# Kernel optimization log

Hardware: AMD Instinct MI355X
Metric: run time of the kernel (lower is better)

The kernel has to match this reference:

```python
import jax, jax.numpy as jnp
import numpy as np

B, L, D, H = 2, 2048, 2048, 16
DH = D // H  # 128 per-head dim
EPS = 1e-5


def setup_inputs() -> dict:
    key = jax.random.key(0)
    ks = jax.random.split(key, 6)
    s = 0.02  # xavier-ish init scale with gain 2**-2.5
    return {
        "hidden_states": jax.random.normal(ks[0], (B, L, D), jnp.float32),
        "Wq": jax.random.normal(ks[1], (D, D), jnp.float32) * s,
        "Wk": jax.random.normal(ks[2], (D, D), jnp.float32) * s,
        "Wv": jax.random.normal(ks[3], (D, D), jnp.float32) * s,
        "Wb": jax.random.normal(ks[4], (D, H), jnp.float32) * s,
        "o_norm_weight": jnp.ones((DH,), jnp.float32),
        "Wo": jax.random.normal(ks[5], (D, D), jnp.float32) * s,
    }


def _delta_rule(q, k, v, beta):
    """Recurrent delta-rule linear attention.
    q,k,v: [B,H,L,Dh]; beta: [B,H,L]. Math identical to fused_chunk_delta_rule.
    S_t = S_{t-1} + k_t (beta_t * (v_t - S_{t-1}^T k_t))^T ;  o_t = S_t^T q_t
    """
    def step(S, inp):
        qt, kt, vt, bt = inp  # [B,H,Dh],[B,H,Dh],[B,H,Dh],[B,H]
        v_pred = jnp.einsum('bhk,bhkv->bhv', kt, S)
        delta = (vt - v_pred) * bt[..., None]
        S = S + kt[..., None] * delta[:, :, None, :]
        ot = jnp.einsum('bhk,bhkv->bhv', qt, S)
        return S, ot

    xs = (q.transpose(2, 0, 1, 3), k.transpose(2, 0, 1, 3),
          v.transpose(2, 0, 1, 3), beta.transpose(2, 0, 1))
    S0 = jnp.zeros(q.shape[:2] + (q.shape[-1], v.shape[-1]), q.dtype)
    _, o = jax.lax.scan(step, S0, xs)  # o: [L,B,H,Dh]
    return o.transpose(1, 2, 0, 3)  # [B,H,L,Dh]


def reference(hidden_states, Wq, Wk, Wv, Wb, o_norm_weight, Wo):
    b, l, d = hidden_states.shape
    h = Wb.shape[1]
    dh = d // h

    q = hidden_states @ Wq
    k = hidden_states @ Wk
    v = jax.nn.silu(hidden_states @ Wv)

    def heads(x):
        return x.reshape(b, l, h, dh).transpose(0, 2, 1, 3)  # b h l d

    q, k, v = heads(q), heads(k), heads(v)

    # qk_norm = 'l2' (torch F.normalize with eps clamp)
    def l2n(x):
        n = jnp.sqrt(jnp.sum(x * x, axis=-1, keepdims=True))
        return x / jnp.maximum(n, 1e-12)

    q, k = l2n(q), l2n(k)
    q = q * (dh ** -0.5)  # fla delta-rule default scale

    beta = jax.nn.sigmoid(hidden_states @ Wb).transpose(0, 2, 1)  # b h l

    o = _delta_rule(q, k, v, beta)  # b h l dh
    o = o.transpose(0, 2, 1, 3)  # b l h dh

    # RMSNorm over head_v_dim
    o = o * jax.lax.rsqrt(jnp.mean(o * o, axis=-1, keepdims=True) + EPS)
    o = o * o_norm_weight

    return o.reshape(b, l, d) @ Wo
```

## Files before the change

### kernel.cpp

```cpp
#include <hip/hip_runtime.h>
#include <hip/hip_bf16.h>
#include <cstdint>

#define DEV static __device__ __forceinline__

typedef unsigned short u16;
typedef unsigned int u32;
typedef __attribute__((ext_vector_type(8))) short short8;
typedef __attribute__((ext_vector_type(4))) float f32x4;

constexpr int Bn = 2, Ln = 2048, Dn = 2048, Hn = 16;
constexpr int Mrows = Bn * Ln;
constexpr int CHK = 64, NCK = Ln / CHK;
constexpr int NCHUNKS = Bn * Hn * NCK;

DEV float b2f(u16 s) { union { float f; u32 u; } x; x.u = ((u32)s) << 16; return x.f; }
DEV u16 f2b(float f) {
  union { float f; u32 u; } x; x.f = f; u32 u = x.u;
  return (u16)((u + 0x7fffu + ((u >> 16) & 1u)) >> 16);
}

DEV void cp16(const void* g, void* l) {
  __builtin_amdgcn_global_load_lds(
      (const __attribute__((address_space(1))) u32*)(unsigned long long)(g),
      (__attribute__((address_space(3))) u32*)(unsigned long long)(l), 16, 0, 0);
}

DEV f32x4 mfma16(short8 a, short8 b, f32x4 c) {
  return __builtin_amdgcn_mfma_f32_16x16x32_bf16(a, b, c, 0, 0, 0);
}

__global__ void k_cvt(const float* __restrict__ src, u16* __restrict__ dst, int n8) {
  int i = blockIdx.x * blockDim.x + threadIdx.x;
  if (i >= n8) return;
  const float4* s4 = (const float4*)(src + (size_t)i * 8);
  float4 a = s4[0], b = s4[1];
  u16 o[8] = {f2b(a.x), f2b(a.y), f2b(a.z), f2b(a.w), f2b(b.x), f2b(b.y), f2b(b.z), f2b(b.w)};
  *(short8*)(dst + (size_t)i * 8) = *(short8*)o;
}

struct TransArgs {
  const float* src[5]; u16* dst[5]; int rows[5]; int cols[5];
};
__global__ void k_trans(TransArgs t) {
  __shared__ u16 tile[32][33];
  int z = blockIdx.z;
  const float* src = t.src[z]; u16* dst = t.dst[z];
  int rows = t.rows[z], cols = t.cols[z];
  int r0 = blockIdx.y * 32, c0 = blockIdx.x * 32;
  if (r0 >= rows || c0 >= cols) return;
  int tx = threadIdx.x, ty = threadIdx.y;
  for (int i = ty; i < 32; i += 8) {
    int r = r0 + i, c = c0 + tx;
    if (r < rows && c < cols) tile[i][tx] = f2b(src[(size_t)r * cols + c]);
  }
  __syncthreads();
  for (int i = ty; i < 32; i += 8) {
    int r = c0 + i, c = r0 + tx;
    if (r < cols && c < rows) dst[(size_t)r * rows + c] = tile[tx][i];
  }
}

__global__ __launch_bounds__(256) void k_beta(const u16* __restrict__ hs,
                                              const u16* __restrict__ WbT,
                                              float* __restrict__ beta_g) {
  int tid = threadIdx.x, wave = tid >> 6, lane = tid & 63, quad = lane >> 4, l15 = lane & 15;
  int tok0 = blockIdx.x * 64 + wave * 16;
  const u16* arow = hs + (size_t)(tok0 + l15) * Dn;
  const u16* brow = WbT + (size_t)l15 * Dn;
  f32x4 acc = {0.f, 0.f, 0.f, 0.f};
  for (int k = 0; k < Dn; k += 32) {
    short8 af = *(const short8*)&arow[k + quad * 8];
    short8 bf = *(const short8*)&brow[k + quad * 8];
    acc = mfma16(af, bf, acc);
  }
  int b = (blockIdx.x * 64) >> 11;
  int l = (blockIdx.x * 64 + wave * 16) & 2047;
#pragma unroll
  for (int r = 0; r < 4; r++) {
    beta_g[(size_t)(b * Hn + l15) * Ln + l + quad * 4 + r] = 1.f / (1.f + __expf(-acc[r]));
  }
}

struct GemmArgs {
  const u16* A; const u16* Bt; void* C; int epi;
  int f32out;
  int M, N, K;
};
__global__ __launch_bounds__(256) void k_gemm(GemmArgs g) {
  __shared__ u16 As[128 * 64];
  __shared__ u16 Bs[128 * 64];
  const u16* A = g.A; const u16* Bt = g.Bt;
  int epi = g.epi;
  int K = g.K, N = g.N;
  int tid = threadIdx.x, wave = tid >> 6, lane = tid & 63;
  int quad = lane >> 4, l15 = lane & 15;
  int m0 = blockIdx.y * 128, n0 = blockIdx.x * 128;
  int wm = (wave >> 1) * 64, wn = (wave & 1) * 64;
  f32x4 acc[4][4];
#pragma unroll
  for (int i = 0; i < 4; i++)
#pragma unroll
    for (int j = 0; j < 4; j++) acc[i][j] = (f32x4){0.f, 0.f, 0.f, 0.f};
  int scol = ((lane & 7) ^ (lane >> 3)) * 8;
  const u16* Ag = A + (size_t)(m0 + wave * 32 + (lane >> 3)) * K + scol;
  const u16* Bg = Bt + (size_t)(n0 + wave * 32 + (lane >> 3)) * K + scol;
  u16* Al = &As[wave * 32 * 64];
  u16* Bl = &Bs[wave * 32 * 64];
  int sw8 = l15 & 7;
  for (int k0 = 0; k0 < K; k0 += 64) {
#pragma unroll
    for (int t = 0; t < 4; t++) {
      cp16(Ag + k0 + t * 8 * K, Al + t * 8 * 64);
      cp16(Bg + k0 + t * 8 * K, Bl + t * 8 * 64);
    }
    __syncthreads();
#pragma unroll
    for (int kk = 0; kk < 64; kk += 32) {
      int sl = (((kk >> 3) + quad) ^ sw8) * 8;
      short8 af[4], bf[4];
#pragma unroll
      for (int i = 0; i < 4; i++) af[i] = *(const short8*)&As[(wm + i * 16 + l15) * 64 + sl];
#pragma unroll
      for (int i = 0; i < 4; i++) bf[i] = *(const short8*)&Bs[(wn + i * 16 + l15) * 64 + sl];
#pragma unroll
      for (int i = 0; i < 4; i++)
#pragma unroll
        for (int j = 0; j < 4; j++) acc[i][j] = mfma16(af[i], bf[j], acc[i][j]);
    }
    __syncthreads();
  }
#pragma unroll
  for (int i = 0; i < 4; i++)
#pragma unroll
    for (int j = 0; j < 4; j++) {
      int row = m0 + wm + i * 16 + quad * 4;
      int col = n0 + wn + j * 16 + l15;
#pragma unroll
      for (int r = 0; r < 4; r++) {
        float v = acc[i][j][r];
        if (epi == 1) v = v / (1.f + __expf(-v));
        if (g.f32out) ((float*)g.C)[(size_t)(row + r) * N + col] = v;
        else ((u16*)g.C)[(size_t)(row + r) * N + col] = f2b(v);
      }
    }
}

struct Gemm2Args { const u16* A; const u16* Bt; u16* C; int K; };

__global__ __launch_bounds__(512, 2) void k_gemm2(Gemm2Args g) {
  __shared__ u16 ldsbuf[61440];
  const char* LB = (const char*)ldsbuf;
  const int K = g.K, NT = K / 64;
  const size_t Kb = (size_t)K * 2;
  int tid = threadIdx.x, wave = tid >> 6, lane = tid & 63;
  int quad = lane >> 4, l15 = lane & 15;
  int wm = wave >> 2, wn = wave & 3;

  int bid = blockIdx.x;
  int wg = (bid & 7) * 32 + (bid >> 3);
  int by = wg >> 4, bx = wg & 15;
  int m0 = by * 256, n0f = bx * 384;

  int r0 = tid >> 2;
  int cby = (((tid & 3) ^ ((tid >> 3) & 3)) * 16);
  const char* gA = (const char*)g.A + (size_t)(m0 + r0) * Kb + cby;
  const char* gB = (const char*)g.Bt + (size_t)(n0f + r0) * Kb + cby;

  auto stageA = [&](int slot, int t, int kh) {
    const char* src = gA + (size_t)t * 128 + kh * 64;
    u16* dst = &ldsbuf[slot * 8192 + tid * 8];
    cp16(src, dst);
    cp16(src + (size_t)128 * Kb, dst + 4096);
  };
  auto stageB = [&](int slot, int t, int kh) {
    const char* src = gB + (size_t)t * 128 + kh * 64;
    u16* dst = &ldsbuf[24576 + slot * 12288 + tid * 8];
    cp16(src, dst);
    cp16(src + (size_t)128 * Kb, dst + 4096);
    cp16(src + (size_t)256 * Kb, dst + 8192);
  };

  f32x4 acc0[4][6], acc1[4][6];
#pragma unroll
  for (int i = 0; i < 4; i++)
#pragma unroll
    for (int j = 0; j < 6; j++) {
      acc0[i][j] = (f32x4){0.f, 0.f, 0.f, 0.f};
      acc1[i][j] = (f32x4){0.f, 0.f, 0.f, 0.f};
    }

  int rsw = (l15 >> 1) & 3;
  int rA = (wm * 128 + l15) * 64 + ((quad ^ rsw) * 16);
  int rB = (wn * 96 + l15) * 64 + ((quad ^ rsw) * 16);

  stageA(0, 0, 0);
  stageB(0, 0, 0);
  stageA(1, 0, 1);
  stageB(1, 0, 1);

  short8 bf[6];
  int u0 = 0;
  for (int t = 0; t < NT; ++t) {
    int u1 = u0 + 1; if (u1 == 3) u1 = 0;
    int u2 = u1 + 1; if (u2 == 3) u2 = 0;
    bool pf = (t + 1 < NT);
    const char* aK0 = LB + u0 * 16384;
    const char* aK1 = LB + u1 * 16384;
    const char* bK0 = LB + 49152 + u0 * 24576;
    const char* bK1 = LB + 49152 + u1 * 24576;

    asm volatile("s_waitcnt vmcnt(5)" ::: "memory");
    __builtin_amdgcn_s_barrier();
    __builtin_amdgcn_sched_barrier(0);
    if (pf) stageA(u2, t + 1, 0);
    {
      short8 av[4];
#pragma unroll
      for (int i = 0; i < 4; i++) av[i] = *(const short8*)(aK0 + rA + i * 1024);
#pragma unroll
      for (int j = 0; j < 6; j++) bf[j] = *(const short8*)(bK0 + rB + j * 1024);
      __builtin_amdgcn_s_setprio(1);
#pragma unroll
      for (int i = 0; i < 4; i++)
#pragma unroll
        for (int j = 0; j < 6; j++) acc0[i][j] = mfma16(av[i], bf[j], acc0[i][j]);
      __builtin_amdgcn_s_setprio(0);
    }

    asm volatile("s_waitcnt vmcnt(5)" ::: "memory");
    __builtin_amdgcn_s_barrier();
    __builtin_amdgcn_sched_barrier(0);
    if (pf) stageB(u2, t + 1, 0);
    {
      short8 av[4];
#pragma unroll
      for (int i = 0; i < 4; i++) av[i] = *(const short8*)(aK0 + rA + 4096 + i * 1024);
      __builtin_amdgcn_s_setprio(1);
#pragma unroll
      for (int i = 0; i < 4; i++)
#pragma unroll
        for (int j = 0; j < 6; j++) acc1[i][j] = mfma16(av[i], bf[j], acc1[i][j]);
      __builtin_amdgcn_s_setprio(0);
    }

    if (t == NT - 1) asm volatile("s_waitcnt vmcnt(0)" ::: "memory");
    else asm volatile("s_waitcnt vmcnt(5)" ::: "memory");
    __builtin_amdgcn_s_barrier();
    __builtin_amdgcn_sched_barrier(0);
    if (pf) stageA(u0, t + 1, 1);
    {
      short8 av[4];
#pragma unroll
      for (int i = 0; i < 4; i++) av[i] = *(const short8*)(aK1 + rA + i * 1024);
#pragma unroll
      for (int j = 0; j < 6; j++) bf[j] = *(const short8*)(bK1 + rB + j * 1024);
      __builtin_amdgcn_s_setprio(1);
#pragma unroll
      for (int i = 0; i < 4; i++)
#pragma unroll
        for (int j = 0; j < 6; j++) acc0[i][j] = mfma16(av[i], bf[j], acc0[i][j]);
      __builtin_amdgcn_s_setprio(0);
    }

    asm volatile("s_waitcnt vmcnt(5)" ::: "memory");
    __builtin_amdgcn_s_barrier();
    __builtin_amdgcn_sched_barrier(0);
    if (pf) stageB(u0, t + 1, 1);
    {
      short8 av[4];
#pragma unroll
      for (int i = 0; i < 4; i++) av[i] = *(const short8*)(aK1 + rA + 4096 + i * 1024);
      __builtin_amdgcn_s_setprio(1);
#pragma unroll
      for (int i = 0; i < 4; i++)
#pragma unroll
        for (int j = 0; j < 6; j++) acc1[i][j] = mfma16(av[i], bf[j], acc1[i][j]);
      __builtin_amdgcn_s_setprio(0);
    }

    u0 = u2;
  }

#pragma unroll
  for (int mq = 0; mq < 2; mq++) {
#pragma unroll
    for (int i = 0; i < 4; i++)
#pragma unroll
      for (int j = 0; j < 6; j++) {
        f32x4 a = mq ? acc1[i][j] : acc0[i][j];
        int row = m0 + wm * 128 + mq * 64 + i * 16 + quad * 4;
        int colg = n0f + wn * 96 + j * 16;
        int z = colg >> 11;
        u16* Cz = g.C + (size_t)z * ((size_t)Mrows * 2048);
        int col = (colg & 2047) + l15;
#pragma unroll
        for (int r = 0; r < 4; r++) {
          float v = a[r];
          if (z == 2) v = v / (1.f + __expf(-v));
          Cz[(size_t)(row + r) * 2048 + col] = f2b(v);
        }
      }
  }
}

__global__ void k_l2(u16* qn, u16* kn) {
  int tid = threadIdx.x, wave = tid >> 6, lane = tid & 63;
  size_t row = (size_t)blockIdx.x * 4 + wave;
  u16* p = (blockIdx.y ? kn : qn) + row * 128;
  u32 u = *(const u32*)&p[lane * 2];
  float x0 = b2f((u16)(u & 0xffff)), x1 = b2f((u16)(u >> 16));
  float ss = x0 * x0 + x1 * x1;
#pragma unroll
  for (int o = 32; o > 0; o >>= 1) ss += __shfl_xor(ss, o, 64);
  float sc = 1.f / fmaxf(sqrtf(ss), 1e-12f);
  if (blockIdx.y == 0) sc *= 0.08838834764831845f;
  u32 outv = (u32)f2b(x0 * sc) | ((u32)f2b(x1 * sc) << 16);
  *(u32*)&p[lane * 2] = outv;
}

constexpr int ST = 72;
__global__ __launch_bounds__(256, 4) void k_pre(
    const float* __restrict__ beta_g,
    const u16* __restrict__ qn, const u16* __restrict__ kn, const u16* __restrict__ vn,
    u16* __restrict__ W2g, u16* __restrict__ Ug, u16* __restrict__ Gg, u16* __restrict__ KTg) {
  __shared__ float beta_s[64];
  __shared__ u16 mats[4 * 64 * ST];
  int gid = blockIdx.x;
  int c = gid & 31, h = (gid >> 5) & 15, b = gid >> 9;
  int tid = threadIdx.x;
  int l0 = c * 64;

  if (tid < 64) beta_s[tid] = beta_g[(size_t)(b * Hn + h) * Ln + l0 + tid];
  __syncthreads();

  int wave = tid >> 6, lane = tid & 63, quad = lane >> 4, l15 = lane & 15;
  u16 *Br = mats, *Bc = mats + 64 * ST, *M0 = mats + 2 * 64 * ST, *M1 = mats + 3 * 64 * ST;

  {
    const u16* krowB = kn + (size_t)(b * Ln + l0 + wave * 16 + l15) * Dn + h * 128;
    short8 bfr[4];
#pragma unroll
    for (int s = 0; s < 4; s++) bfr[s] = *(const short8*)&krowB[quad * 8 + 32 * s];
#pragma unroll
    for (int mt = 0; mt < 4; ++mt) {
      const u16* arow_k = kn + (size_t)(b * Ln + l0 + mt * 16 + l15) * Dn + h * 128;
      const u16* arow_q = qn + (size_t)(b * Ln + l0 + mt * 16 + l15) * Dn + h * 128;
      f32x4 accA = {0.f, 0.f, 0.f, 0.f}, accG = {0.f, 0.f, 0.f, 0.f};
#pragma unroll
      for (int s = 0; s < 4; s++) {
        short8 ak = *(const short8*)&arow_k[quad * 8 + 32 * s];
        short8 aq = *(const short8*)&arow_q[quad * 8 + 32 * s];
        accA = mfma16(ak, bfr[s], accA);
        accG = mfma16(aq, bfr[s], accG);
      }
      int t = wave * 16 + l15;
#pragma unroll
      for (int r = 0; r < 4; r++) {
        int i = mt * 16 + quad * 4 + r;
        u16 nb = f2b((t < i) ? -beta_s[i] * accA[r] : 0.f);
        Br[i * ST + t] = nb;
        Bc[t * ST + i] = nb;
        M0[i * ST + t] = (t == i) ? f2b(1.f) : nb;
        Gg[(size_t)gid * 4096 + (size_t)i * 64 + t] = f2b((t <= i) ? accG[r] : 0.f);
      }
    }
  }
  __syncthreads();

  u16 *Mc = M0, *Mn = M1;
#pragma unroll
  for (int it = 0; it < 5; ++it) {
    const int tT = (it < 3) ? 0 : ((it == 3) ? 1 : 2);
    const int tI = (it < 4) ? 0 : 1;
    short8 bb[2];
#pragma unroll
    for (int s = 0; s < 2; s++) bb[s] = *(const short8*)&Bc[(wave * 16 + l15) * ST + quad * 8 + 32 * s];
    f32x4 accT[4];
#pragma unroll
    for (int mt = 0; mt < 4; mt++) {
      accT[mt] = (f32x4){0.f, 0.f, 0.f, 0.f};
      if (mt - wave >= tT) {
#pragma unroll
        for (int s = 0; s < 2; s++) {
          short8 af = *(const short8*)&Br[(mt * 16 + l15) * ST + quad * 8 + 32 * s];
          accT[mt] = mfma16(af, bb[s], accT[mt]);
        }
      }
    }
    __syncthreads();
#pragma unroll
    for (int mt = 0; mt < 4; mt++) {
      if (mt - wave >= tI) {
#pragma unroll
        for (int r = 0; r < 4; r++) {
          int i = mt * 16 + quad * 4 + r, t = wave * 16 + l15;
          u16 v = f2b(accT[mt][r]);
          Br[i * ST + t] = v;
          Bc[t * ST + i] = v;
        }
      }
    }
    __syncthreads();
    short8 tb[2];
#pragma unroll
    for (int s = 0; s < 2; s++) tb[s] = *(const short8*)&Bc[(wave * 16 + l15) * ST + quad * 8 + 32 * s];
#pragma unroll
    for (int mt = 0; mt < 4; mt++) {
      if (mt - wave >= tT) {
        f32x4 a;
#pragma unroll
        for (int r = 0; r < 4; r++) a[r] = b2f(Mc[(mt * 16 + quad * 4 + r) * ST + wave * 16 + l15]);
#pragma unroll
        for (int s = 0; s < 2; s++) {
          short8 af = *(const short8*)&Mc[(mt * 16 + l15) * ST + quad * 8 + 32 * s];
          a = mfma16(af, tb[s], a);
        }
#pragma unroll
        for (int r = 0; r < 4; r++) Mn[(mt * 16 + quad * 4 + r) * ST + wave * 16 + l15] = f2b(a[r]);
      } else {
#pragma unroll
        for (int r = 0; r < 4; r++)
          Mn[(mt * 16 + quad * 4 + r) * ST + wave * 16 + l15] =
              Mc[(mt * 16 + quad * 4 + r) * ST + wave * 16 + l15];
      }
    }
    u16* tmp = Mc; Mc = Mn; Mn = tmp;
  }
  __syncthreads();

  u16* XT = mats;
  for (int pass = 0; pass < 2; ++pass) {
    const u16* src = pass ? vn : kn;
    for (int idx = tid; idx < 64 * 128; idx += 256) {
      int t = idx >> 7, dk = idx & 127;
      float v = b2f(src[(size_t)(b * Ln + l0 + t) * Dn + h * 128 + dk]);
      XT[dk * ST + t] = f2b(v * beta_s[t]);
      if (pass == 0) KTg[(size_t)gid * 8192 + (size_t)dk * 64 + t] = f2b(v);
    }
    __syncthreads();
    u16* dst = pass ? Ug : W2g;
#pragma unroll
    for (int half = 0; half < 2; ++half) {
      int nt = wave + half * 4;
      short8 bx[2];
#pragma unroll
      for (int s = 0; s < 2; s++) bx[s] = *(const short8*)&XT[(nt * 16 + l15) * ST + quad * 8 + 32 * s];
#pragma unroll
      for (int mt = 0; mt < 4; mt++) {
        f32x4 a = {0.f, 0.f, 0.f, 0.f};
#pragma unroll
        for (int s = 0; s < 2; s++) {
          short8 af = *(const short8*)&Mc[(mt * 16 + l15) * ST + quad * 8 + 32 * s];
          a = mfma16(af, bx[s], a);
        }
#pragma unroll
        for (int r = 0; r < 4; r++)
          dst[(size_t)gid * 8192 + (size_t)(mt * 16 + quad * 4 + r) * 128 + nt * 16 + l15] = f2b(a[r]);
      }
    }
    __syncthreads();
  }
}

struct Frg { short8 w2[4], qf[4], gf[2], k0[2], k1[2]; float u[4]; };

__global__ __launch_bounds__(256) void k_scan(
    const u16* __restrict__ qn, const u16* __restrict__ W2g, const u16* __restrict__ Ug,
    const u16* __restrict__ Gg, const u16* __restrict__ KTg, u16* __restrict__ Og) {
  constexpr int SST = 136, DST = 104;
  __shared__ u16 Sb[16 * SST];
  __shared__ u16 Db[16 * DST];
  int bh = blockIdx.x, sl = blockIdx.y;
  int b = bh >> 4, h = bh & 15, c0 = sl * 16;
  int tid = threadIdx.x, wave = tid >> 6, lane = tid & 63, quad = lane >> 4, l15 = lane & 15;
  for (int i = tid; i < 16 * SST; i += 256) Sb[i] = 0;
  f32x4 accS0 = {0.f, 0.f, 0.f, 0.f}, accS1 = {0.f, 0.f, 0.f, 0.f};
  __syncthreads();

  auto load_frags = [&](Frg& F, int ci) {
    size_t ck = (size_t)bh * NCK + ci;
    const u16* w2row = W2g + ck * 8192 + (size_t)(wave * 16 + l15) * 128;
    const u16* qrow = qn + (size_t)(b * Ln + ci * 64 + wave * 16 + l15) * Dn + h * 128;
#pragma unroll
    for (int s = 0; s < 4; s++) {
      F.w2[s] = *(const short8*)&w2row[quad * 8 + 32 * s];
      F.qf[s] = *(const short8*)&qrow[quad * 8 + 32 * s];
    }
    const u16* grow = Gg + ck * 4096 + (size_t)(wave * 16 + l15) * 64;
    const u16* kt0 = KTg + ck * 8192 + (size_t)(wave * 16 + l15) * 64;
    const u16* kt1 = KTg + ck * 8192 + (size_t)((wave + 4) * 16 + l15) * 64;
#pragma unroll
    for (int s = 0; s < 2; s++) {
      F.gf[s] = *(const short8*)&grow[quad * 8 + 32 * s];
      F.k0[s] = *(const short8*)&kt0[quad * 8 + 32 * s];
      F.k1[s] = *(const short8*)&kt1[quad * 8 + 32 * s];
    }
    const u16* urow = Ug + ck * 8192 + (size_t)(wave * 16 + quad * 4) * 128 + c0 + l15;
#pragma unroll
    for (int r = 0; r < 4; r++) F.u[r] = b2f(urow[(size_t)r * 128]);
  };

  auto compute = [&](const Frg& F, int ci) {
    f32x4 accT = {0.f, 0.f, 0.f, 0.f}, accO = {0.f, 0.f, 0.f, 0.f};
#pragma unroll
    for (int s = 0; s < 4; s++) {
      short8 sf = *(const short8*)&Sb[l15 * SST + quad * 8 + 32 * s];
      accT = mfma16(F.w2[s], sf, accT);
      accO = mfma16(F.qf[s], sf, accO);
    }
#pragma unroll
    for (int r = 0; r < 4; r++) {
      float d = F.u[r] - accT[r];
      Db[l15 * DST + wave * 16 + quad * 4 + r] = f2b(d);
    }
    __syncthreads();
#pragma unroll
    for (int s = 0; s < 2; s++) {
      short8 df = *(const short8*)&Db[l15 * DST + quad * 8 + 32 * s];
      accO = mfma16(F.gf[s], df, accO);
      accS0 = mfma16(F.k0[s], df, accS0);
      accS1 = mfma16(F.k1[s], df, accS1);
    }
    u16* orow = Og + (size_t)(b * Ln + ci * 64 + wave * 16 + quad * 4) * Dn + h * 128 + c0 + l15;
#pragma unroll
    for (int r = 0; r < 4; r++) orow[(size_t)r * Dn] = f2b(accO[r]);
#pragma unroll
    for (int r = 0; r < 4; r++) {
      Sb[l15 * SST + wave * 16 + quad * 4 + r] = f2b(accS0[r]);
      Sb[l15 * SST + (wave + 4) * 16 + quad * 4 + r] = f2b(accS1[r]);
    }
    __syncthreads();
  };

  Frg FA, FB;
  load_frags(FA, 0);
  for (int ci = 0; ci < NCK; ci += 2) {
    load_frags(FB, ci + 1);
    compute(FA, ci);
    if (ci + 2 < NCK) load_frags(FA, ci + 2);
    compute(FB, ci + 1);
  }
}

__global__ void k_rms(const u16* __restrict__ Og, const float* __restrict__ w, u16* __restrict__ out) {
  int tid = threadIdx.x, wave = tid >> 6, lane = tid & 63;
  size_t row = (size_t)blockIdx.x * 4 + wave;
  const u16* p = Og + row * 128;
  u32 u = *(const u32*)&p[lane * 2];
  float x0 = b2f((u16)(u & 0xffff)), x1 = b2f((u16)(u >> 16));
  float ss = x0 * x0 + x1 * x1;
#pragma unroll
  for (int o = 32; o > 0; o >>= 1) ss += __shfl_xor(ss, o, 64);
  float sc = rsqrtf(ss * (1.f / 128.f) + 1e-5f);
  float w0 = w[lane * 2], w1 = w[lane * 2 + 1];
  u32 o2 = (u32)f2b(x0 * sc * w0) | ((u32)f2b(x1 * sc * w1) << 16);
  *(u32*)&out[row * 128 + lane * 2] = o2;
}

extern "C" void kernel_launch(void* const* d_in, const int* in_sizes, int n_in,
                              void* d_out, int out_size, void* d_ws, size_t ws_size,
                              hipStream_t stream) {
  (void)in_sizes; (void)n_in; (void)out_size; (void)ws_size;
  const float* hs_f = (const float*)d_in[0];
  const float* Wq = (const float*)d_in[1];
  const float* Wk = (const float*)d_in[2];
  const float* Wv = (const float*)d_in[3];
  const float* Wb = (const float*)d_in[4];
  const float* onw = (const float*)d_in[5];
  const float* Wo = (const float*)d_in[6];

  char* ws = (char*)d_ws;
  size_t off = 0;
  auto alloc = [&](size_t bytes) -> void* {
    void* p = ws + off;
    off += (bytes + 255) & ~(size_t)255;
    return p;
  };
  const size_t WB = (size_t)2048 * 2048 * 2;
  const size_t XB = (size_t)4096 * 2048 * 2;
  u16* WqT = (u16*)alloc(WB);
  u16* WkT = (u16*)alloc(WB);
  u16* WvT = (u16*)alloc(WB);
  u16* WoT = (u16*)alloc(WB);
  u16* WbT = (u16*)alloc((size_t)16 * 2048 * 2);
  u16* hsb = (u16*)alloc(XB);
  u16* qn  = (u16*)alloc(XB);
  u16* kn  = (u16*)alloc(XB);
  u16* vn  = (u16*)alloc(XB);
  u16* W2g = (u16*)alloc((size_t)NCHUNKS * 8192 * 2);
  u16* Ug  = (u16*)alloc((size_t)NCHUNKS * 8192 * 2);
  u16* Gg  = (u16*)alloc((size_t)NCHUNKS * 4096 * 2);
  u16* KTg = (u16*)alloc((size_t)NCHUNKS * 8192 * 2);
  float* beta_g = (float*)alloc((size_t)Bn * Hn * Ln * 4);
  u16* Og = vn;
  u16* onorm = qn;

  hipLaunchKernelGGL(k_cvt, dim3(Mrows * Dn / 8 / 256), dim3(256), 0, stream, hs_f, hsb, Mrows * Dn / 8);

  TransArgs ta;
  ta.src[0] = Wq; ta.dst[0] = WqT; ta.rows[0] = 2048; ta.cols[0] = 2048;
  ta.src[1] = Wk; ta.dst[1] = WkT; ta.rows[1] = 2048; ta.cols[1] = 2048;
  ta.src[2] = Wv; ta.dst[2] = WvT; ta.rows[2] = 2048; ta.cols[2] = 2048;
  ta.src[3] = Wo; ta.dst[3] = WoT; ta.rows[3] = 2048; ta.cols[3] = 2048;
  ta.src[4] = Wb; ta.dst[4] = WbT; ta.rows[4] = 2048; ta.cols[4] = 16;
  hipLaunchKernelGGL(k_trans, dim3(64, 64, 5), dim3(32, 8), 0, stream, ta);

  hipLaunchKernelGGL(k_beta, dim3(Mrows / 64), dim3(256), 0, stream, hsb, WbT, beta_g);

  {
    Gemm2Args g2;
    g2.A = hsb; g2.Bt = WqT; g2.C = qn; g2.K = 2048;
    hipLaunchKernelGGL(k_gemm2, dim3(256), dim3(512), 0, stream, g2);
  }

  hipLaunchKernelGGL(k_l2, dim3(16384, 2), dim3(256), 0, stream, qn, kn);

  hipLaunchKernelGGL(k_pre, dim3(NCHUNKS), dim3(256), 0, stream,
                     beta_g, qn, kn, vn, W2g, Ug, Gg, KTg);

  hipLaunchKernelGGL(k_scan, dim3(32, 8), dim3(256), 0, stream,
                     qn, W2g, Ug, Gg, KTg, Og);

  hipLaunchKernelGGL(k_rms, dim3(16384), dim3(256), 0, stream, Og, onw, onorm);

  GemmArgs go;
  go.A = onorm; go.Bt = WoT; go.C = d_out; go.epi = 0;
  go.f32out = 1; go.M = Mrows; go.N = 2048; go.K = 2048;
  hipLaunchKernelGGL(k_gemm, dim3(16, 32), dim3(256), 0, stream, go);
}
```

Measured before the change: 488.3 us.

## Halve barriers per K step in QKV GEMM by merging A/B prefetch phases

Restructures the QKV projection GEMM main loop so each half-K phase reads its A and B fragments from LDS, then issues both the A and B prefetch for the next step and runs both MFMA halves. There is one wait-plus-barrier at the end of each phase instead of one before each quarter. This halves the number of workgroup barriers per K iteration and lets the global prefetch overlap more MFMA work. In exchange, more global loads are in flight at each barrier, and the vmcnt(5) accounting has to stay correct for the larger issue groups.

```diff
diff --git a/kernel.cpp b/kernel.cpp
--- a/kernel.cpp
+++ b/kernel.cpp
@@ -194,92 +194,57 @@
   int rA = (wm * 128 + l15) * 64 + ((quad ^ rsw) * 16);
   int rB = (wn * 96 + l15) * 64 + ((quad ^ rsw) * 16);
 
-  stageA(0, 0, 0);
-  stageB(0, 0, 0);
-  stageA(1, 0, 1);
-  stageB(1, 0, 1);
-
-  short8 bf[6];
-  int u0 = 0;
+  stageA(0, 0, 0); stageB(0, 0, 0);
+  stageA(1, 0, 1); stageB(1, 0, 1);
+  asm volatile("s_waitcnt vmcnt(5)" ::: "memory");
+  __builtin_amdgcn_s_barrier();
+  asm volatile("" ::: "memory");
+  __builtin_amdgcn_sched_barrier(0);
+
+  auto phase = [&](int rc, int rs, int kh, int t, bool pf) {
+    const char* aK = LB + rc * 16384;
+    const char* bK = LB + 49152 + rc * 24576;
+    short8 bfv[6], av[4];
+#pragma unroll
+    for (int j = 0; j < 6; j++) bfv[j] = *(const short8*)(bK + rB + j * 1024);
+#pragma unroll
+    for (int i = 0; i < 4; i++) av[i] = *(const short8*)(aK + rA + i * 1024);
+    if (pf) { stageA(rs, t + 1, kh); stageB(rs, t + 1, kh); }
+    __builtin_amdgcn_s_setprio(1);
+#pragma unroll
+    for (int i = 0; i < 4; i++)
+#pragma unroll
+      for (int j = 0; j < 6; j++) acc0[i][j] = mfma16(av[i], bfv[j], acc0[i][j]);
+    __builtin_amdgcn_s_setprio(0);
+#pragma unroll
+    for (int i = 0; i < 4; i++) av[i] = *(const short8*)(aK + rA + 4096 + i * 1024);
+    __builtin_amdgcn_s_setprio(1);
+#pragma unroll
+    for (int i = 0; i < 4; i++)
+#pragma unroll
+      for (int j = 0; j < 6; j++) acc1[i][j] = mfma16(av[i], bfv[j], acc1[i][j]);
+    __builtin_amdgcn_s_setprio(0);
+    if (pf) {
+      asm volatile("s_waitcnt vmcnt(5)" ::: "memory");
+      __builtin_amdgcn_s_barrier();
+      asm volatile("" ::: "memory");
+      __builtin_amdgcn_sched_barrier(0);
+    } else if (kh == 0) {
+      asm volatile("s_waitcnt vmcnt(0)" ::: "memory");
+      __builtin_amdgcn_s_barrier();
+      asm volatile("" ::: "memory");
+      __builtin_amdgcn_sched_barrier(0);
+    }
+  };
+
+  int r = 0;
   for (int t = 0; t < NT; ++t) {
-    int u1 = u0 + 1; if (u1 == 3) u1 = 0;
-    int u2 = u1 + 1; if (u2 == 3) u2 = 0;
+    int r1 = r + 1; if (r1 == 3) r1 = 0;
+    int r2 = r1 + 1; if (r2 == 3) r2 = 0;
     bool pf = (t + 1 < NT);
-    const char* aK0 = LB + u0 * 16384;
-    const char* aK1 = LB + u1 * 16384;
-    const char* bK0 = LB + 49152 + u0 * 24576;
-    const char* bK1 = LB + 49152 + u1 * 24576;
-
-    asm volatile("s_waitcnt vmcnt(5)" ::: "memory");
-    __builtin_amdgcn_s_barrier();
-    __builtin_amdgcn_sched_barrier(0);
-    if (pf) stageA(u2, t + 1, 0);
-    {
-      short8 av[4];
-#pragma unroll
-      for (int i = 0; i < 4; i++) av[i] = *(const short8*)(aK0 + rA + i * 1024);
-#pragma unroll
-      for (int j = 0; j < 6; j++) bf[j] = *(const short8*)(bK0 + rB + j * 1024);
-      __builtin_amdgcn_s_setprio(1);
-#pragma unroll
-      for (int i = 0; i < 4; i++)
-#pragma unroll
-        for (int j = 0; j < 6; j++) acc0[i][j] = mfma16(av[i], bf[j], acc0[i][j]);
-      __builtin_amdgcn_s_setprio(0);
-    }
-
-    asm volatile("s_waitcnt vmcnt(5)" ::: "memory");
-    __builtin_amdgcn_s_barrier();
-    __builtin_amdgcn_sched_barrier(0);
-    if (pf) stageB(u2, t + 1, 0);
-    {
-      short8 av[4];
-#pragma unroll
-      for (int i = 0; i < 4; i++) av[i] = *(const short8*)(aK0 + rA + 4096 + i * 1024);
-      __builtin_amdgcn_s_setprio(1);
-#pragma unroll
-      for (int i = 0; i < 4; i++)
-#pragma unroll
-        for (int j = 0; j < 6; j++) acc1[i][j] = mfma16(av[i], bf[j], acc1[i][j]);
-      __builtin_amdgcn_s_setprio(0);
-    }
-
-    if (t == NT - 1) asm volatile("s_waitcnt vmcnt(0)" ::: "memory");
-    else asm volatile("s_waitcnt vmcnt(5)" ::: "memory");
-    __builtin_amdgcn_s_barrier();
-    __builtin_amdgcn_sched_barrier(0);
-    if (pf) stageA(u0, t + 1, 1);
-    {
-      short8 av[4];
-#pragma unroll
-      for (int i = 0; i < 4; i++) av[i] = *(const short8*)(aK1 + rA + i * 1024);
-#pragma unroll
-      for (int j = 0; j < 6; j++) bf[j] = *(const short8*)(bK1 + rB + j * 1024);
-      __builtin_amdgcn_s_setprio(1);
-#pragma unroll
-      for (int i = 0; i < 4; i++)
-#pragma unroll
-        for (int j = 0; j < 6; j++) acc0[i][j] = mfma16(av[i], bf[j], acc0[i][j]);
-      __builtin_amdgcn_s_setprio(0);
-    }
-
-    asm volatile("s_waitcnt vmcnt(5)" ::: "memory");
-    __builtin_amdgcn_s_barrier();
-    __builtin_amdgcn_sched_barrier(0);
-    if (pf) stageB(u0, t + 1, 1);
-    {
-      short8 av[4];
-#pragma unroll
-      for (int i = 0; i < 4; i++) av[i] = *(const short8*)(aK1 + rA + 4096 + i * 1024);
-      __builtin_amdgcn_s_setprio(1);
-#pragma unroll
-      for (int i = 0; i < 4; i++)
-#pragma unroll
-        for (int j = 0; j < 6; j++) acc1[i][j] = mfma16(av[i], bf[j], acc1[i][j]);
-      __builtin_amdgcn_s_setprio(0);
-    }
-
-    u0 = u2;
+    phase(r, r2, 0, t, pf);
+    phase(r1, r, 1, t, pf);
+    r = r2;
   }
 
 #pragma unroll
@@ -295,10 +260,10 @@
         u16* Cz = g.C + (size_t)z * ((size_t)Mrows * 2048);
         int col = (colg & 2047) + l15;
 #pragma unroll
-        for (int r = 0; r < 4; r++) {
-          float v = a[r];
+        for (int r2_ = 0; r2_ < 4; r2_++) {
+          float v = a[r2_];
           if (z == 2) v = v / (1.f + __expf(-v));
-          Cz[(size_t)(row + r) * 2048 + col] = f2b(v);
+          Cz[(size_t)(row + r2_) * 2048 + col] = f2b(v);
         }
       }
   }
```

Measured after the change: 526.9 us. +7.9%, slower.
